# Optimization experiments

Hardware: AMD Instinct MI355X
Metric: run time of the kernel (lower is better)

## Reference

```python
import jax, jax.numpy as jnp
import numpy as np

EPS = 1e-5
K = 20

def knn_idx(x, k):
    # x: (B, N, C). Torch computes -||xi-xj||^2 and takes topk (largest => nearest).
    xx = jnp.sum(x * x, axis=-1)                      # (B, N)
    inner = jnp.einsum('bnc,bmc->bnm', x, x)          # (B, N, N)
    neg_dist = 2.0 * inner - xx[:, :, None] - xx[:, None, :]
    return jax.lax.top_k(neg_dist, k)[1]              # (B, N, k) int32

def edge_feature(x, k):
    # x: (B, N, C) -> (B, N, k, 2C) = concat(neighbor - center, center)
    B = x.shape[0]
    idx = knn_idx(x, k)
    nb = x[jnp.arange(B)[:, None, None], idx]         # (B, N, k, C) gather
    ctr = jnp.broadcast_to(x[:, :, None, :], nb.shape)
    return jnp.concatenate([nb - ctr, ctr], axis=-1)

def batchnorm(x, gamma, beta, axes):
    # training-mode BN over `axes` (per-channel on last axis)
    m = jnp.mean(x, axis=axes, keepdims=True)
    v = jnp.var(x, axis=axes, keepdims=True)
    return (x - m) * jax.lax.rsqrt(v + EPS) * gamma + beta

def lrelu(x):
    return jnp.where(x >= 0, x, 0.2 * x)

def conv_bn_act(x, w, g, b):
    # 1x1 conv on (B, N, k, Cin) with weight (Cout, Cin), BN over (B, N, k)
    y = jnp.einsum('bnkc,oc->bnko', x, w)
    return lrelu(batchnorm(y, g, b, (0, 1, 2)))


def setup_inputs() -> dict:
    key = jax.random.key(0)
    ks = jax.random.split(key, 16)
    B, N = 4, 4096
    d = {'x': jax.random.normal(ks[0], (B, 3, N), dtype=jnp.float32)}
    d['w1'] = jax.random.normal(ks[1], (64, 6),    dtype=jnp.float32) * 0.1
    d['w2'] = jax.random.normal(ks[2], (64, 64),   dtype=jnp.float32) * 0.1
    d['w3'] = jax.random.normal(ks[3], (64, 128),  dtype=jnp.float32) * 0.1
    d['w4'] = jax.random.normal(ks[4], (64, 64),   dtype=jnp.float32) * 0.1
    d['w5'] = jax.random.normal(ks[5], (64, 128),  dtype=jnp.float32) * 0.1
    d['w6'] = jax.random.normal(ks[6], (1024, 192), dtype=jnp.float32) * 0.05
    d['wl'] = jax.random.normal(ks[7], (512, 1024), dtype=jnp.float32) * 0.05
    for i, c in zip(range(1, 8), [64, 64, 64, 64, 64, 1024, 512]):
        d[f'g{i}'] = jnp.ones((c,), jnp.float32)
        d[f'b{i}'] = jnp.zeros((c,), jnp.float32)
    return d


def reference(x, w1, w2, w3, w4, w5, w6, wl,
              g1, b1, g2, b2, g3, b3, g4, b4, g5, b5, g6, b6, g7, b7):
    p = jnp.transpose(x[:, :3, :], (0, 2, 1))         # (B, N, 3)
    # EdgeConv block 1
    e = edge_feature(p, K)                            # (B, N, k, 6)
    h = conv_bn_act(e, w1, g1, b1)
    h = conv_bn_act(h, w2, g2, b2)
    x1 = jnp.max(h, axis=2)                           # (B, N, 64)
    # EdgeConv block 2
    e = edge_feature(x1, K)                           # (B, N, k, 128)
    h = conv_bn_act(e, w3, g3, b3)
    h = conv_bn_act(h, w4, g4, b4)
    x2 = jnp.max(h, axis=2)
    # EdgeConv block 3
    e = edge_feature(x2, K)
    h = conv_bn_act(e, w5, g5, b5)
    x3 = jnp.max(h, axis=2)
    # point-wise 1x1 conv to 1024 then global max pool
    cat = jnp.concatenate([x1, x2, x3], axis=-1)      # (B, N, 192)
    h = lrelu(batchnorm(jnp.einsum('bnc,oc->bno', cat, w6), g6, b6, (0, 1)))
    g = jnp.max(h, axis=1)                            # (B, 1024)
    out = batchnorm(g @ wl.T, g7, b7, (0,))           # (B, 512)
    return out
```

## Files before the change

### kernel.cpp

```cpp
#include <hip/hip_runtime.h>

static constexpr int PB  = 4;
static constexpr int PN  = 4096;
static constexpr int PK  = 20;
static constexpr int PNT = PB*PN*PK;
#define NEGF (-3.402823466e38f)

__device__ __forceinline__ float lrelu_f(float x){ return x >= 0.f ? x : 0.2f*x; }

#define FMA4C(accv, av, bv) { accv = fmaf((av).x,(bv).x,accv); accv = fmaf((av).y,(bv).y,accv); \
                              accv = fmaf((av).z,(bv).z,accv); accv = fmaf((av).w,(bv).w,accv); }

__global__ __launch_bounds__(512) void k_knn3(const float* __restrict__ x, int* __restrict__ idxb){
  __shared__ float4 pts[PN];
  int t = threadIdx.x;
  int b = blockIdx.y;
  const float* xb = x + (size_t)b*3*PN;
  for(int i=t;i<PN;i+=512){
    float a0 = xb[i], a1 = xb[PN+i], a2 = xb[2*PN+i];
    float s = a0*a0; s = fmaf(a1,a1,s); s = fmaf(a2,a2,s);
    pts[i] = make_float4(a0,a1,a2,s);
  }
  __syncthreads();
  int lane = t & 63, w = t >> 6;
  int row = blockIdx.x*8 + w;
  float4 pi = pts[row];
  unsigned long long removed = 0ull;

#define KDIST(E) ({ float4 pj_ = pts[lane + ((E)<<6)]; \
    float dt_ = pi.x*pj_.x; dt_ = fmaf(pi.y,pj_.y,dt_); dt_ = fmaf(pi.z,pj_.z,dt_); \
    fmaf(2.f,dt_,-pi.w) - pj_.w; })

  float gv0,gv1,gv2,gv3,gv4,gv5,gv6,gv7;
  int   gi0,gi1,gi2,gi3,gi4,gi5,gi6,gi7;
#define KBUILDG(G) { float gm_=NEGF; int ge_=(G)*8; \
    _Pragma("unroll") for(int e_=(G)*8; e_<(G)*8+8; e_++){ \
      bool ok_ = ((removed >> e_) & 1ull) == 0ull; \
      float d_ = KDIST(e_); \
      bool bt_ = ok_ && (d_ > gm_); gm_ = bt_ ? d_ : gm_; ge_ = bt_ ? e_ : ge_; } \
    gv##G = gm_; gi##G = ge_; }
  KBUILDG(0) KBUILDG(1) KBUILDG(2) KBUILDG(3) KBUILDG(4) KBUILDG(5) KBUILDG(6) KBUILDG(7)

  float lmax; int le;
#define KLBEST { lmax = gv0; le = gi0; \
    if(gv1>lmax){lmax=gv1;le=gi1;} if(gv2>lmax){lmax=gv2;le=gi2;} \
    if(gv3>lmax){lmax=gv3;le=gi3;} if(gv4>lmax){lmax=gv4;le=gi4;} \
    if(gv5>lmax){lmax=gv5;le=gi5;} if(gv6>lmax){lmax=gv6;le=gi6;} \
    if(gv7>lmax){lmax=gv7;le=gi7;} }
  KLBEST

  int myidx = 0;
  for(int k=0;k<PK;k++){
    float g = lmax;
    #pragma unroll
    for(int s=32;s>=1;s>>=1) g = fmaxf(g, __shfl_xor(g, s));
    unsigned long long cand = __ballot(lmax == g);
    int jw;
    if(__popcll(cand) == 1){
      int wl = __ffsll(cand) - 1;
      int e  = __shfl(le, wl);
      jw = wl + (e<<6);
    } else {
      unsigned jj = (lmax == g) ? (unsigned)(lane + (le<<6)) : 0xFFFFFFFFu;
      #pragma unroll
      for(int s=32;s>=1;s>>=1){ unsigned o = __shfl_xor(jj, s); jj = (o < jj) ? o : jj; }
      jw = (int)jj;
    }
    if(lane == k) myidx = jw;
    if((jw & 63) == lane){
      int e = jw >> 6;
      removed |= (1ull << e);
      int q = e >> 3;
      if(q==0){ KBUILDG(0) } else if(q==1){ KBUILDG(1) }
      else if(q==2){ KBUILDG(2) } else if(q==3){ KBUILDG(3) }
      else if(q==4){ KBUILDG(4) } else if(q==5){ KBUILDG(5) }
      else if(q==6){ KBUILDG(6) } else { KBUILDG(7) }
      KLBEST
    }
  }
  if(lane < PK) idxb[((size_t)b*PN + row)*PK + lane] = myidx;
#undef KDIST
#undef KBUILDG
#undef KLBEST
}

__global__ __launch_bounds__(256) void k_dist64(const float* __restrict__ Xb, const float* __restrict__ xxb,
                                                float* __restrict__ D){
  __shared__ float Xi[128*32];
  __shared__ float Xj[128*32];
  __shared__ float xxi[128], xxj[128];
  int t = threadIdx.x;
  int p = blockIdx.x;
  int bi = (int)((65.0f - sqrtf(4225.0f - 8.0f*(float)p)) * 0.5f);
  while((bi+1)*32 - ((bi+1)*bi)/2 <= p) bi++;
  while(bi*32 - (bi*(bi-1))/2 > p) bi--;
  int bj = bi + (p - (bi*32 - (bi*(bi-1))/2));
  int i0 = bi*128, j0 = bj*128;
  int prg = t>>4, cq = t&15;
  float acc[8][8];
  #pragma unroll
  for(int pp=0;pp<8;pp++)
    #pragma unroll
    for(int oc=0;oc<8;oc++) acc[pp][oc] = 0.f;

  for(int h=0;h<2;h++){
    if(h) __syncthreads();
    #pragma unroll
    for(int k=0;k<4;k++){
      int fid = t + k*256; int row = fid>>3, c4 = fid&7;
      ((float4*)Xi)[row*8 + (c4^(row&7))] = ((const float4*)(Xb + (size_t)(i0+row)*64 + h*32))[c4];
      ((float4*)Xj)[row*8 + (c4^(row&7))] = ((const float4*)(Xb + (size_t)(j0+row)*64 + h*32))[c4];
    }
    if(h==0){
      if(t < 128) xxi[t] = xxb[i0+t];
      else        xxj[t-128] = xxb[j0+t-128];
    }
    __syncthreads();
    #pragma unroll 4
    for(int c4=0;c4<8;c4++){
      float4 a[8], bb[8];
      #pragma unroll
      for(int pp=0;pp<8;pp++){ int row = prg*8+pp; a[pp] = ((const float4*)Xi)[row*8 + (c4^(row&7))]; }
      #pragma unroll
      for(int oc=0;oc<8;oc++){ int col = cq+16*oc;  bb[oc] = ((const float4*)Xj)[col*8 + (c4^(col&7))]; }
      #pragma unroll
      for(int pp=0;pp<8;pp++)
        #pragma unroll
        for(int oc=0;oc<8;oc++) FMA4C(acc[pp][oc], a[pp], bb[oc]);
    }
  }
  #pragma unroll
  for(int pp=0;pp<8;pp++){
    int r = prg*8+pp;
    float xi2 = xxi[r];
    float* Drow = D + (size_t)(i0+r)*PN + j0;
    #pragma unroll
    for(int oc=0;oc<8;oc++){
      int c = cq + 16*oc;
      Drow[c] = fmaf(2.f, acc[pp][oc], -xi2) - xxj[c];
    }
  }
  if(bi != bj){
    #pragma unroll
    for(int oc=0;oc<8;oc++){
      int c = cq + 16*oc;
      float xj2 = xxj[c];
      float* Dcol = D + (size_t)(j0+c)*PN + i0 + prg*8;
      float4 t0, t1;
      t0.x = fmaf(2.f, acc[0][oc], -xj2) - xxi[prg*8+0];
      t0.y = fmaf(2.f, acc[1][oc], -xj2) - xxi[prg*8+1];
      t0.z = fmaf(2.f, acc[2][oc], -xj2) - xxi[prg*8+2];
      t0.w = fmaf(2.f, acc[3][oc], -xj2) - xxi[prg*8+3];
      t1.x = fmaf(2.f, acc[4][oc], -xj2) - xxi[prg*8+4];
      t1.y = fmaf(2.f, acc[5][oc], -xj2) - xxi[prg*8+5];
      t1.z = fmaf(2.f, acc[6][oc], -xj2) - xxi[prg*8+6];
      t1.w = fmaf(2.f, acc[7][oc], -xj2) - xxi[prg*8+7];
      ((float4*)Dcol)[0] = t0;
      ((float4*)Dcol)[1] = t1;
    }
  }
}

__global__ __launch_bounds__(256) void k_topk(const float* __restrict__ D, int* __restrict__ idxb){
  int t = threadIdx.x, lane = t & 63, w = t >> 6;
  int row = blockIdx.x*4 + w;
  const float4* rp = (const float4*)(D + (size_t)row*PN + lane*64);
  float v[64];
  #pragma unroll
  for(int c=0;c<16;c++){
    float4 q = rp[c];
    v[4*c+0]=q.x; v[4*c+1]=q.y; v[4*c+2]=q.z; v[4*c+3]=q.w;
  }
  float gv0,gv1,gv2,gv3,gv4,gv5,gv6,gv7;
  int   gi0,gi1,gi2,gi3,gi4,gi5,gi6,gi7;
#define TBUILDG(G) { float gm_=NEGF; int ge_=(G)*8; \
    _Pragma("unroll") for(int e_=(G)*8; e_<(G)*8+8; e_++){ \
      bool bt_ = v[e_] > gm_; gm_ = bt_ ? v[e_] : gm_; ge_ = bt_ ? e_ : ge_; } \
    gv##G = gm_; gi##G = ge_; }
#define TPOIS(G) { _Pragma("unroll") for(int e_=(G)*8; e_<(G)*8+8; e_++){ \
      if(e_ == rel) v[e_] = NEGF; } }
  TBUILDG(0) TBUILDG(1) TBUILDG(2) TBUILDG(3) TBUILDG(4) TBUILDG(5) TBUILDG(6) TBUILDG(7)
  float lmax; int li;
#define TLBEST { lmax = gv0; li = gi0; \
    if(gv1>lmax){lmax=gv1;li=gi1;} if(gv2>lmax){lmax=gv2;li=gi2;} \
    if(gv3>lmax){lmax=gv3;li=gi3;} if(gv4>lmax){lmax=gv4;li=gi4;} \
    if(gv5>lmax){lmax=gv5;li=gi5;} if(gv6>lmax){lmax=gv6;li=gi6;} \
    if(gv7>lmax){lmax=gv7;li=gi7;} }
  TLBEST
  int myidx = 0;
  for(int k=0;k<PK;k++){
    float g = lmax;
    #pragma unroll
    for(int s=32;s>=1;s>>=1) g = fmaxf(g, __shfl_xor(g, s));
    unsigned long long mask = __ballot(lmax == g);
    int wl = __ffsll((unsigned long long)mask) - 1;
    int rel = __shfl(li, wl);
    if(lane == k) myidx = wl*64 + rel;
    if(lane == wl){
      int q = rel >> 3;
      if(q==0){ TPOIS(0) TBUILDG(0) } else if(q==1){ TPOIS(1) TBUILDG(1) }
      else if(q==2){ TPOIS(2) TBUILDG(2) } else if(q==3){ TPOIS(3) TBUILDG(3) }
      else if(q==4){ TPOIS(4) TBUILDG(4) } else if(q==5){ TPOIS(5) TBUILDG(5) }
      else if(q==6){ TPOIS(6) TBUILDG(6) } else { TPOIS(7) TBUILDG(7) }
      TLBEST
    }
  }
  if(lane < PK) idxb[row*PK + lane] = myidx;
#undef TBUILDG
#undef TPOIS
#undef TLBEST
}

__global__ __launch_bounds__(256) void k_nodeUV3(const float* __restrict__ x, const float* __restrict__ w1,
                                                 float* __restrict__ U, float* __restrict__ V){
  __shared__ float ww[384];
  int t = threadIdx.x;
  for(int k=t;k<384;k+=256) ww[k] = w1[k];
  __syncthreads();
  int g = blockIdx.x*256 + t;
  int ng = g >> 6, o = g & 63;
  int b = ng >> 12, n = ng & 4095;
  const float* xb = x + (size_t)b*3*PN;
  float p0 = xb[n], p1 = xb[PN+n], p2 = xb[2*PN+n];
  const float* wr = ww + o*6;
  float u = p0*wr[0]; u = fmaf(p1,wr[1],u); u = fmaf(p2,wr[2],u);
  float vv = p0*(wr[3]-wr[0]); vv = fmaf(p1, wr[4]-wr[1], vv); vv = fmaf(p2, wr[5]-wr[2], vv);
  U[(size_t)ng*64+o] = u;
  V[(size_t)ng*64+o] = vv;
}

__global__ __launch_bounds__(256) void k_nodeUV64(const float* __restrict__ xf, const float* __restrict__ w,
                                                  float* __restrict__ U, float* __restrict__ V){
  __shared__ float xbuf[128*64];
  __shared__ float wbuf[128*64];
  int t = threadIdx.x;
  int r0 = blockIdx.x * 128;
  #pragma unroll
  for(int k=0;k<8;k++){
    int fid = t + k*256; int row = fid>>4, c4 = fid&15;
    ((float4*)xbuf)[row*16 + (c4^(row&15))] = ((const float4*)(xf + (size_t)(r0+row)*64))[c4];
    float4 wv;
    if(row < 64){
      wv = ((const float4*)(w + (size_t)row*128))[c4];
    } else {
      float4 w2v = ((const float4*)(w + (size_t)(row-64)*128 + 64))[c4];
      float4 w1v = ((const float4*)(w + (size_t)(row-64)*128))[c4];
      wv.x = w2v.x-w1v.x; wv.y = w2v.y-w1v.y; wv.z = w2v.z-w1v.z; wv.w = w2v.w-w1v.w;
    }
    ((float4*)wbuf)[row*16 + (c4^(row&15))] = wv;
  }
  __syncthreads();
  int rg = t>>4, cq = t&15;
  float acc[8][8];
  #pragma unroll
  for(int pp=0;pp<8;pp++)
    #pragma unroll
    for(int oc=0;oc<8;oc++) acc[pp][oc] = 0.f;
  #pragma unroll 4
  for(int c4=0;c4<16;c4++){
    float4 a[8], bb[8];
    #pragma unroll
    for(int pp=0;pp<8;pp++){ int row = rg*8+pp; a[pp] = ((const float4*)xbuf)[row*16 + (c4^(row&15))]; }
    #pragma unroll
    for(int oc=0;oc<8;oc++){ int col = cq+16*oc;  bb[oc] = ((const float4*)wbuf)[col*16 + (c4^(col&15))]; }
    #pragma unroll
    for(int pp=0;pp<8;pp++)
      #pragma unroll
      for(int oc=0;oc<8;oc++) FMA4C(acc[pp][oc], a[pp], bb[oc]);
  }
  #pragma unroll
  for(int pp=0;pp<8;pp++){
    int r = r0 + rg*8+pp;
    #pragma unroll
    for(int oc=0;oc<8;oc++){
      int col = cq + 16*oc;
      if(col < 64) U[(size_t)r*64 + col] = acc[pp][oc];
      else         V[(size_t)r*64 + col-64] = acc[pp][oc];
    }
  }
}

__global__ __launch_bounds__(256) void k_statUV(const float* __restrict__ U, const float* __restrict__ V,
                                                const int* __restrict__ idx, float* __restrict__ part){
  __shared__ float4 sArr[256];
  __shared__ float4 qArr[256];
  int t = threadIdx.x; int blk = blockIdx.x;
  int ch4 = t & 15, sub = t >> 4;
  int qbase = blk*640;
  float4 s = make_float4(0,0,0,0), qq = make_float4(0,0,0,0);
  for(int r=sub; r<640; r+=16){
    int q = qbase + r;
    int pt = q/PK;
    int b = pt >> 12;
    int j = idx[q];
    float4 u4 = ((const float4*)(U + (size_t)(b*PN+j)*64))[ch4];
    float4 v4 = ((const float4*)(V + (size_t)pt*64))[ch4];
    float4 y4;
    y4.x = u4.x+v4.x; y4.y = u4.y+v4.y; y4.z = u4.z+v4.z; y4.w = u4.w+v4.w;
    s.x += y4.x; s.y += y4.y; s.z += y4.z; s.w += y4.w;
    qq.x = fmaf(y4.x,y4.x,qq.x); qq.y = fmaf(y4.y,y4.y,qq.y);
    qq.z = fmaf(y4.z,y4.z,qq.z); qq.w = fmaf(y4.w,y4.w,qq.w);
  }
  sArr[t] = s; qArr[t] = qq;
  __syncthreads();
  if(t < 16){
    float4 S = make_float4(0,0,0,0), Q = make_float4(0,0,0,0);
    #pragma unroll
    for(int g=0;g<16;g++){
      float4 a = sArr[g*16 + t], b = qArr[g*16 + t];
      S.x+=a.x; S.y+=a.y; S.z+=a.z; S.w+=a.w;
      Q.x+=b.x; Q.y+=b.y; Q.z+=b.z; Q.w+=b.w;
    }
    ((float4*)(part + (size_t)blk*128))[t] = S;
    ((float4*)(part + (size_t)blk*128 + 64))[t] = Q;
  }
}

__global__ __launch_bounds__(256) void k_convAF(const float* __restrict__ U, const float* __restrict__ V,
                                                const int* __restrict__ idx, const float* __restrict__ wg,
                                                const float* __restrict__ sb, float* __restrict__ y,
                                                float* __restrict__ part){
  __shared__ float hbuf[128*64];
  __shared__ float wbuf[64*64];
  int t = threadIdx.x;
  int q0 = blockIdx.x * 128;
  #pragma unroll
  for(int k=0;k<8;k++){
    int fid = t + k*256; int row = fid>>4, c4 = fid&15;
    int q = q0 + row;
    int pt = q/PK; int b = pt>>12; int j = idx[q];
    float4 uu = ((const float4*)(U + (size_t)(b*PN+j)*64))[c4];
    float4 vv = ((const float4*)(V + (size_t)pt*64))[c4];
    float4 sc = ((const float4*)sb)[c4];
    float4 bi = ((const float4*)(sb+1024))[c4];
    float4 h;
    h.x = lrelu_f(fmaf(uu.x+vv.x, sc.x, bi.x));
    h.y = lrelu_f(fmaf(uu.y+vv.y, sc.y, bi.y));
    h.z = lrelu_f(fmaf(uu.z+vv.z, sc.z, bi.z));
    h.w = lrelu_f(fmaf(uu.w+vv.w, sc.w, bi.w));
    ((float4*)hbuf)[row*16 + (c4 ^ (row&15))] = h;
  }
  #pragma unroll
  for(int k=0;k<4;k++){
    int fid = t + k*256; int row = fid>>4, c4 = fid&15;
    ((float4*)wbuf)[row*16 + (c4 ^ (row&15))] = ((const float4*)(wg + row*64))[c4];
  }
  __syncthreads();
  int prg = t >> 4, cq = t & 15;
  float acc[8][4];
  #pragma unroll
  for(int pp=0;pp<8;pp++)
    #pragma unroll
    for(int oc=0;oc<4;oc++) acc[pp][oc] = 0.f;
  #pragma unroll 4
  for(int c4=0;c4<16;c4++){
    float4 a[8], b4[4];
    #pragma unroll
    for(int pp=0;pp<8;pp++){ int row = prg*8+pp; a[pp] = ((const float4*)hbuf)[row*16 + (c4^(row&15))]; }
    #pragma unroll
    for(int oc=0;oc<4;oc++){ int och = cq + 16*oc; b4[oc] = ((const float4*)wbuf)[och*16 + (c4^(och&15))]; }
    #pragma unroll
    for(int pp=0;pp<8;pp++)
      #pragma unroll
      for(int oc=0;oc<4;oc++) FMA4C(acc[pp][oc], a[pp], b4[oc]);
  }
  #pragma unroll
  for(int pp=0;pp<8;pp++)
    #pragma unroll
    for(int oc=0;oc<4;oc++)
      y[(size_t)(q0 + prg*8+pp)*64 + cq + 16*oc] = acc[pp][oc];

  float s_[4], q_[4];
  #pragma unroll
  for(int oc=0;oc<4;oc++){
    float s = 0.f, q = 0.f;
    #pragma unroll
    for(int pp=0;pp<8;pp++){ s += acc[pp][oc]; q = fmaf(acc[pp][oc], acc[pp][oc], q); }
    s_[oc] = s; q_[oc] = q;
  }
  __syncthreads();
  float* ls = wbuf;
  #pragma unroll
  for(int oc=0;oc<4;oc++){
    ls[(cq + 16*oc)*16 + prg]        = s_[oc];
    ls[2048 + (cq + 16*oc)*16 + prg] = q_[oc];
  }
  __syncthreads();
  if(t < 64){
    float S = 0.f, Q = 0.f;
    #pragma unroll
    for(int g=0;g<16;g++){ S += ls[t*16+g]; Q += ls[2048 + t*16+g]; }
    part[(size_t)blockIdx.x*128 + t] = S;
    part[(size_t)blockIdx.x*128 + 64 + t] = Q;
  }
}

__global__ __launch_bounds__(256) void k_red1024(const float* __restrict__ y6, float* __restrict__ part){
  int t = threadIdx.x; int blk = blockIdx.x;
  const float4* base = (const float4*)(y6 + (size_t)blk*128*1024);
  float4 s = make_float4(0,0,0,0), q = make_float4(0,0,0,0);
  for(int r=0;r<128;r++){
    float4 v = base[r*256 + t];
    s.x += v.x; s.y += v.y; s.z += v.z; s.w += v.w;
    q.x = fmaf(v.x,v.x,q.x); q.y = fmaf(v.y,v.y,q.y); q.z = fmaf(v.z,v.z,q.z); q.w = fmaf(v.w,v.w,q.w);
  }
  ((float4*)(part + (size_t)blk*2048))[t] = s;
  ((float4*)(part + (size_t)blk*2048 + 1024))[t] = q;
}

__global__ __launch_bounds__(256) void k_fin(const float* __restrict__ part, int nparts, int chn, float cnt,
                                             const float* __restrict__ gamma, const float* __restrict__ beta,
                                             float* __restrict__ sb){
  __shared__ float ls[512];
  int t = threadIdx.x;
  int chl = t & 15, sub = t >> 4;
  int ch = blockIdx.x*16 + chl;
  float S = 0.f, Q = 0.f;
  for(int p=sub; p<nparts; p+=16){
    S += part[(size_t)p*2*chn + ch];
    Q += part[(size_t)p*2*chn + chn + ch];
  }
  ls[t] = S; ls[256+t] = Q;
  __syncthreads();
  if(t < 16){
    float Sa = 0.f, Qa = 0.f;
    #pragma unroll
    for(int s=0;s<16;s++){ Sa += ls[s*16+t]; Qa += ls[256+s*16+t]; }
    int c = blockIdx.x*16 + t;
    float m  = Sa/cnt;
    float vr = Qa/cnt - m*m;
    float sc = gamma[c] * rsqrtf(vr + 1e-5f);
    sb[c] = sc; sb[1024+c] = beta[c] - m*sc;
  }
}

__global__ __launch_bounds__(256) void k_finish(const float* __restrict__ y, const float* __restrict__ sb,
                                                float* __restrict__ xo, float* __restrict__ xxo){
  __shared__ float ls[256];
  int t = threadIdx.x;
  int pt = blockIdx.x*16 + (t>>4), c4 = t&15;
  const float4* base = (const float4*)(y + (size_t)pt*20*64);
  float4 sc = ((const float4*)sb)[c4];
  float4 bi = ((const float4*)(sb+1024))[c4];
  float4 m = make_float4(NEGF,NEGF,NEGF,NEGF);
  #pragma unroll 4
  for(int k=0;k<20;k++){
    float4 v = base[k*16 + c4];
    v.x = lrelu_f(fmaf(v.x, sc.x, bi.x)); v.y = lrelu_f(fmaf(v.y, sc.y, bi.y));
    v.z = lrelu_f(fmaf(v.z, sc.z, bi.z)); v.w = lrelu_f(fmaf(v.w, sc.w, bi.w));
    m.x = fmaxf(m.x,v.x); m.y = fmaxf(m.y,v.y); m.z = fmaxf(m.z,v.z); m.w = fmaxf(m.w,v.w);
  }
  ((float4*)(xo + (size_t)pt*64))[c4] = m;
  float ss = m.x*m.x; ss = fmaf(m.y,m.y,ss); ss = fmaf(m.z,m.z,ss); ss = fmaf(m.w,m.w,ss);
  ls[t] = ss;
  __syncthreads();
  if(c4 == 0){
    float S = 0.f;
    #pragma unroll
    for(int c=0;c<16;c++) S += ls[(t & 0xF0) + c];
    xxo[pt] = S;
  }
}

__global__ __launch_bounds__(256) void k_finishUV(const float* __restrict__ U, const float* __restrict__ V,
                                                  const int* __restrict__ idx, const float* __restrict__ sb,
                                                  float* __restrict__ xo){
  int t = threadIdx.x;
  int pt = blockIdx.x*16 + (t>>4), c4 = t&15;
  int b = pt >> 12;
  float4 sc = ((const float4*)sb)[c4];
  float4 bi = ((const float4*)(sb+1024))[c4];
  float4 vv = ((const float4*)(V + (size_t)pt*64))[c4];
  float4 m = make_float4(NEGF,NEGF,NEGF,NEGF);
  const int* ip = idx + (size_t)pt*PK;
  #pragma unroll 4
  for(int k=0;k<PK;k++){
    int j = ip[k];
    float4 uu = ((const float4*)(U + (size_t)(b*PN+j)*64))[c4];
    float4 v;
    v.x = lrelu_f(fmaf(uu.x+vv.x, sc.x, bi.x)); v.y = lrelu_f(fmaf(uu.y+vv.y, sc.y, bi.y));
    v.z = lrelu_f(fmaf(uu.z+vv.z, sc.z, bi.z)); v.w = lrelu_f(fmaf(uu.w+vv.w, sc.w, bi.w));
    m.x = fmaxf(m.x,v.x); m.y = fmaxf(m.y,v.y); m.z = fmaxf(m.z,v.z); m.w = fmaxf(m.w,v.w);
  }
  ((float4*)(xo + (size_t)pt*64))[c4] = m;
}

__global__ __launch_bounds__(256) void k_gemm6(const float* __restrict__ x1, const float* __restrict__ x2,
                                               const float* __restrict__ x3, const float* __restrict__ w6,
                                               float* __restrict__ y6){
  __shared__ float cb[128*64];
  __shared__ float wb[128*64];
  int t = threadIdx.x;
  int rb = blockIdx.x >> 3;
  int ob = blockIdx.x & 7;
  size_t r0 = (size_t)rb*128; int o0 = ob*128;
  int prg = t >> 4, cq = t & 15;
  float acc[8][8];
  #pragma unroll
  for(int pp=0;pp<8;pp++)
    #pragma unroll
    for(int oc=0;oc<8;oc++) acc[pp][oc] = 0.f;
  const float* srcs[3] = {x1, x2, x3};
  for(int ph=0; ph<3; ph++){
    __syncthreads();
    const float* src = srcs[ph];
    #pragma unroll
    for(int k=0;k<8;k++){
      int fid = t + k*256; int row = fid>>4, c4 = fid&15;
      ((float4*)cb)[row*16 + (c4^(row&15))] = ((const float4*)(src + (r0+row)*64))[c4];
      ((float4*)wb)[row*16 + (c4^(row&15))] = ((const float4*)(w6 + (size_t)(o0+row)*192 + ph*64))[c4];
    }
    __syncthreads();
    #pragma unroll 4
    for(int c4=0;c4<16;c4++){
      float4 a[8], b8[8];
      #pragma unroll
      for(int pp=0;pp<8;pp++){ int row = prg*8+pp; a[pp] = ((const float4*)cb)[row*16 + (c4^(row&15))]; }
      #pragma unroll
      for(int oc=0;oc<8;oc++){ int och = cq + 16*oc; b8[oc] = ((const float4*)wb)[och*16 + (c4^(och&15))]; }
      #pragma unroll
      for(int pp=0;pp<8;pp++)
        #pragma unroll
        for(int oc=0;oc<8;oc++) FMA4C(acc[pp][oc], a[pp], b8[oc]);
    }
  }
  #pragma unroll
  for(int pp=0;pp<8;pp++)
    #pragma unroll
    for(int oc=0;oc<8;oc++)
      y6[(r0 + prg*8+pp)*1024 + o0 + cq + 16*oc] = acc[pp][oc];
}

__global__ __launch_bounds__(256) void k_gmax(const float* __restrict__ y6, const float* __restrict__ sb,
                                              float* __restrict__ gpart){
  int t = threadIdx.x; int blk = blockIdx.x;
  const float4* base = (const float4*)(y6 + (size_t)blk*256*1024);
  float4 sc = ((const float4*)sb)[t];
  float4 bi = ((const float4*)(sb+1024))[t];
  float4 m = make_float4(NEGF,NEGF,NEGF,NEGF);
  for(int r=0;r<256;r++){
    float4 v = base[r*256 + t];
    v.x = lrelu_f(fmaf(v.x, sc.x, bi.x)); v.y = lrelu_f(fmaf(v.y, sc.y, bi.y));
    v.z = lrelu_f(fmaf(v.z, sc.z, bi.z)); v.w = lrelu_f(fmaf(v.w, sc.w, bi.w));
    m.x = fmaxf(m.x,v.x); m.y = fmaxf(m.y,v.y); m.z = fmaxf(m.z,v.z); m.w = fmaxf(m.w,v.w);
  }
  ((float4*)(gpart + (size_t)blk*1024))[t] = m;
}

__global__ __launch_bounds__(256) void k_gmaxfin(const float* __restrict__ gpart, float* __restrict__ g){
  int b = blockIdx.x, t = threadIdx.x;
  float4 m = make_float4(NEGF,NEGF,NEGF,NEGF);
  for(int c=0;c<16;c++){
    float4 v = ((const float4*)(gpart + ((size_t)b*16 + c)*1024))[t];
    m.x = fmaxf(m.x,v.x); m.y = fmaxf(m.y,v.y); m.z = fmaxf(m.z,v.z); m.w = fmaxf(m.w,v.w);
  }
  ((float4*)(g + (size_t)b*1024))[t] = m;
}

__global__ __launch_bounds__(256) void k_final(const float* __restrict__ g, const float* __restrict__ wl,
                                               const float* __restrict__ g7, const float* __restrict__ b7,
                                               float* __restrict__ out){
  int gt = blockIdx.x*256 + threadIdx.x;
  int o = gt >> 2, b = gt & 3;
  const float4* gb = (const float4*)(g + (size_t)b*1024);
  const float4* wr = (const float4*)(wl + (size_t)o*1024);
  float acc = 0.f;
  #pragma unroll 4
  for(int c=0;c<256;c++){
    float4 a = gb[c], w = wr[c];
    acc = fmaf(a.x,w.x,acc); acc = fmaf(a.y,w.y,acc);
    acc = fmaf(a.z,w.z,acc); acc = fmaf(a.w,w.w,acc);
  }
  float s = acc + __shfl_xor(acc, 1);
  s = s + __shfl_xor(s, 2);
  float m = s * 0.25f;
  float d = acc - m;
  float vv = d*d;
  float v2 = vv + __shfl_xor(vv, 1);
  v2 = v2 + __shfl_xor(v2, 2);
  float var = v2 * 0.25f;
  out[b*512 + o] = d * rsqrtf(var + 1e-5f) * g7[o] + b7[o];
}

extern "C" void kernel_launch(void* const* d_in, const int* in_sizes, int n_in,
                              void* d_out, int out_size, void* d_ws, size_t ws_size,
                              hipStream_t stream){
  const float* x  = (const float*)d_in[0];
  const float* w1 = (const float*)d_in[1];
  const float* w2 = (const float*)d_in[2];
  const float* w3 = (const float*)d_in[3];
  const float* w4 = (const float*)d_in[4];
  const float* w5 = (const float*)d_in[5];
  const float* w6 = (const float*)d_in[6];
  const float* wl = (const float*)d_in[7];
  const float* g1 = (const float*)d_in[8];  const float* b1 = (const float*)d_in[9];
  const float* g2 = (const float*)d_in[10]; const float* b2 = (const float*)d_in[11];
  const float* g3 = (const float*)d_in[12]; const float* b3 = (const float*)d_in[13];
  const float* g4 = (const float*)d_in[14]; const float* b4 = (const float*)d_in[15];
  const float* g5 = (const float*)d_in[16]; const float* b5 = (const float*)d_in[17];
  const float* g6 = (const float*)d_in[18]; const float* b6 = (const float*)d_in[19];
  const float* g7 = (const float*)d_in[20]; const float* b7 = (const float*)d_in[21];
  float* out = (float*)d_out;

  float* ws    = (float*)d_ws;
  float* xx    = ws;
  int*   idx   = (int*)(ws + 16384);
  float* y     = ws + 344064;
  float* Dbuf  = y;
  float* x1    = ws + 21315584;
  float* x2    = x1 + 1048576;
  float* x3    = x2 + 1048576;
  float* part  = x3 + 1048576;
  float* sb    = part + 327680;
  float* gpart = sb + 2048;
  float* g     = gpart + 65536;
  float* U     = g + 4096;
  float* V     = U + 1048576;

  k_knn3<<<dim3(512,4),512,0,stream>>>(x, idx);
  k_nodeUV3<<<4096,256,0,stream>>>(x, w1, U, V);
  k_statUV<<<512,256,0,stream>>>(U, V, idx, part);
  k_fin<<<4,256,0,stream>>>(part, 512, 64, (float)PNT, g1, b1, sb);
  k_convAF<<<2560,256,0,stream>>>(U, V, idx, w2, sb, y, part);
  k_fin<<<4,256,0,stream>>>(part, 2560, 64, (float)PNT, g2, b2, sb);
  k_finish<<<1024,256,0,stream>>>(y, sb, x1, xx);

  for(int b=0;b<PB;b++){
    k_dist64<<<528,256,0,stream>>>(x1 + (size_t)b*PN*64, xx + b*PN, Dbuf);
    k_topk<<<1024,256,0,stream>>>(Dbuf, idx + (size_t)b*PN*PK);
  }
  k_nodeUV64<<<128,256,0,stream>>>(x1, w3, U, V);
  k_statUV<<<512,256,0,stream>>>(U, V, idx, part);
  k_fin<<<4,256,0,stream>>>(part, 512, 64, (float)PNT, g3, b3, sb);
  k_convAF<<<2560,256,0,stream>>>(U, V, idx, w4, sb, y, part);
  k_fin<<<4,256,0,stream>>>(part, 2560, 64, (float)PNT, g4, b4, sb);
  k_finish<<<1024,256,0,stream>>>(y, sb, x2, xx);

  for(int b=0;b<PB;b++){
    k_dist64<<<528,256,0,stream>>>(x2 + (size_t)b*PN*64, xx + b*PN, Dbuf);
    k_topk<<<1024,256,0,stream>>>(Dbuf, idx + (size_t)b*PN*PK);
  }
  k_nodeUV64<<<128,256,0,stream>>>(x2, w5, U, V);
  k_statUV<<<512,256,0,stream>>>(U, V, idx, part);
  k_fin<<<4,256,0,stream>>>(part, 512, 64, (float)PNT, g5, b5, sb);
  k_finishUV<<<1024,256,0,stream>>>(U, V, idx, sb, x3);

  k_gemm6<<<1024,256,0,stream>>>(x1, x2, x3, w6, y);
  k_red1024<<<128,256,0,stream>>>(y, part);
  k_fin<<<64,256,0,stream>>>(part, 128, 1024, 16384.f, g6, b6, sb);
  k_gmax<<<64,256,0,stream>>>(y, sb, gpart);
  k_gmaxfin<<<4,256,0,stream>>>(gpart, g);
  k_final<<<8,256,0,stream>>>(g, wl, g7, b7, out);
}
```

Before: 1.245 ms.

## Use split-bf16 MFMA for the 64x64 edge conv GEMM in k_convAF

Replaces the scalar FP32 FMA inner product in k_convAF with bf16 MFMA instructions (16x16x32). Inputs and weights are split into hi and lo bf16 parts and combined with three MFMAs per tile, which approximates FP32 accuracy. Shared-memory staging changes to a swizzled bf16 layout. The goal is to offload the GEMM to the matrix cores, at the cost of extra conversion work and slightly lower precision than true FP32.

Result: faster. 1.199 ms (-3.7%).

```diff
diff --git a/kernel.cpp b/kernel.cpp
--- a/kernel.cpp
+++ b/kernel.cpp
@@ -7,6 +7,16 @@
 #define NEGF (-3.402823466e38f)
 
 __device__ __forceinline__ float lrelu_f(float x){ return x >= 0.f ? x : 0.2f*x; }
+
+typedef __attribute__((ext_vector_type(8))) short short8v;
+typedef __attribute__((ext_vector_type(4))) float f32x4;
+
+__device__ __forceinline__ unsigned short f2bf(float f){
+  unsigned u = __float_as_uint(f);
+  unsigned r = u + 0x7FFFu + ((u>>16)&1u);
+  return (unsigned short)(r>>16);
+}
+__device__ __forceinline__ float bf2f(unsigned short s){ return __uint_as_float(((unsigned)s)<<16); }
 
 #define FMA4C(accv, av, bv) { accv = fmaf((av).x,(bv).x,accv); accv = fmaf((av).y,(bv).y,accv); \
                               accv = fmaf((av).z,(bv).z,accv); accv = fmaf((av).w,(bv).w,accv); }
@@ -320,8 +330,8 @@
                                                 const int* __restrict__ idx, const float* __restrict__ wg,
                                                 const float* __restrict__ sb, float* __restrict__ y,
                                                 float* __restrict__ part){
-  __shared__ float hbuf[128*64];
-  __shared__ float wbuf[64*64];
+  __shared__ short hb[2*128*64];
+  __shared__ short wb[2*64*64];
   int t = threadIdx.x;
   int q0 = blockIdx.x * 128;
   #pragma unroll
@@ -338,52 +348,95 @@
     h.y = lrelu_f(fmaf(uu.y+vv.y, sc.y, bi.y));
     h.z = lrelu_f(fmaf(uu.z+vv.z, sc.z, bi.z));
     h.w = lrelu_f(fmaf(uu.w+vv.w, sc.w, bi.w));
-    ((float4*)hbuf)[row*16 + (c4 ^ (row&15))] = h;
+    int base = row*64 + ((((c4>>1) ^ (row&7)))<<3) + ((c4&1)<<2);
+    short4 hi4, lo4;
+    hi4.x = (short)f2bf(h.x); lo4.x = (short)f2bf(h.x - bf2f((unsigned short)hi4.x));
+    hi4.y = (short)f2bf(h.y); lo4.y = (short)f2bf(h.y - bf2f((unsigned short)hi4.y));
+    hi4.z = (short)f2bf(h.z); lo4.z = (short)f2bf(h.z - bf2f((unsigned short)hi4.z));
+    hi4.w = (short)f2bf(h.w); lo4.w = (short)f2bf(h.w - bf2f((unsigned short)hi4.w));
+    *(short4*)(hb + base) = hi4;
+    *(short4*)(hb + 8192 + base) = lo4;
   }
   #pragma unroll
   for(int k=0;k<4;k++){
     int fid = t + k*256; int row = fid>>4, c4 = fid&15;
-    ((float4*)wbuf)[row*16 + (c4 ^ (row&15))] = ((const float4*)(wg + row*64))[c4];
-  }
-  __syncthreads();
-  int prg = t >> 4, cq = t & 15;
-  float acc[8][4];
-  #pragma unroll
-  for(int pp=0;pp<8;pp++)
-    #pragma unroll
-    for(int oc=0;oc<4;oc++) acc[pp][oc] = 0.f;
-  #pragma unroll 4
-  for(int c4=0;c4<16;c4++){
-    float4 a[8], b4[4];
-    #pragma unroll
-    for(int pp=0;pp<8;pp++){ int row = prg*8+pp; a[pp] = ((const float4*)hbuf)[row*16 + (c4^(row&15))]; }
-    #pragma unroll
-    for(int oc=0;oc<4;oc++){ int och = cq + 16*oc; b4[oc] = ((const float4*)wbuf)[och*16 + (c4^(och&15))]; }
-    #pragma unroll
-    for(int pp=0;pp<8;pp++)
-      #pragma unroll
-      for(int oc=0;oc<4;oc++) FMA4C(acc[pp][oc], a[pp], b4[oc]);
-  }
-  #pragma unroll
-  for(int pp=0;pp<8;pp++)
-    #pragma unroll
-    for(int oc=0;oc<4;oc++)
-      y[(size_t)(q0 + prg*8+pp)*64 + cq + 16*oc] = acc[pp][oc];
-
-  float s_[4], q_[4];
-  #pragma unroll
-  for(int oc=0;oc<4;oc++){
-    float s = 0.f, q = 0.f;
-    #pragma unroll
-    for(int pp=0;pp<8;pp++){ s += acc[pp][oc]; q = fmaf(acc[pp][oc], acc[pp][oc], q); }
-    s_[oc] = s; q_[oc] = q;
-  }
-  __syncthreads();
-  float* ls = wbuf;
-  #pragma unroll
-  for(int oc=0;oc<4;oc++){
-    ls[(cq + 16*oc)*16 + prg]        = s_[oc];
-    ls[2048 + (cq + 16*oc)*16 + prg] = q_[oc];
+    float4 wv = ((const float4*)(wg + (size_t)row*64))[c4];
+    int base = row*64 + ((((c4>>1) ^ (row&7)))<<3) + ((c4&1)<<2);
+    short4 hi4, lo4;
+    hi4.x = (short)f2bf(wv.x); lo4.x = (short)f2bf(wv.x - bf2f((unsigned short)hi4.x));
+    hi4.y = (short)f2bf(wv.y); lo4.y = (short)f2bf(wv.y - bf2f((unsigned short)hi4.y));
+    hi4.z = (short)f2bf(wv.z); lo4.z = (short)f2bf(wv.z - bf2f((unsigned short)hi4.z));
+    hi4.w = (short)f2bf(wv.w); lo4.w = (short)f2bf(wv.w - bf2f((unsigned short)hi4.w));
+    *(short4*)(wb + base) = hi4;
+    *(short4*)(wb + 4096 + base) = lo4;
+  }
+  __syncthreads();
+
+  int lane = t & 63, w = t >> 6;
+  int r0w = w*32;
+  short8v ah[2][2], al[2][2];
+  #pragma unroll
+  for(int rt=0;rt<2;rt++)
+    #pragma unroll
+    for(int kc=0;kc<2;kc++){
+      int row = r0w + rt*16 + (lane&15);
+      int kb  = kc*4 + (lane>>4);
+      int off = row*64 + ((kb ^ (row&7))<<3);
+      ah[rt][kc] = *(const short8v*)(hb + off);
+      al[rt][kc] = *(const short8v*)(hb + 8192 + off);
+    }
+  short8v bh[4][2], bl[4][2];
+  #pragma unroll
+  for(int ct=0;ct<4;ct++)
+    #pragma unroll
+    for(int kc=0;kc<2;kc++){
+      int o   = ct*16 + (lane&15);
+      int kb  = kc*4 + (lane>>4);
+      int off = o*64 + ((kb ^ (o&7))<<3);
+      bh[ct][kc] = *(const short8v*)(wb + off);
+      bl[ct][kc] = *(const short8v*)(wb + 4096 + off);
+    }
+
+  f32x4 acc[2][4];
+  #pragma unroll
+  for(int rt=0;rt<2;rt++)
+    #pragma unroll
+    for(int ct=0;ct<4;ct++)
+      acc[rt][ct] = (f32x4){0.f,0.f,0.f,0.f};
+
+  #pragma unroll
+  for(int rt=0;rt<2;rt++)
+    #pragma unroll
+    for(int ct=0;ct<4;ct++)
+      #pragma unroll
+      for(int kc=0;kc<2;kc++){
+        acc[rt][ct] = __builtin_amdgcn_mfma_f32_16x16x32_bf16(ah[rt][kc], bh[ct][kc], acc[rt][ct], 0,0,0);
+        acc[rt][ct] = __builtin_amdgcn_mfma_f32_16x16x32_bf16(ah[rt][kc], bl[ct][kc], acc[rt][ct], 0,0,0);
+        acc[rt][ct] = __builtin_amdgcn_mfma_f32_16x16x32_bf16(al[rt][kc], bh[ct][kc], acc[rt][ct], 0,0,0);
+      }
+
+  float s_[4] = {0.f,0.f,0.f,0.f}, q_[4] = {0.f,0.f,0.f,0.f};
+  #pragma unroll
+  for(int rt=0;rt<2;rt++)
+    #pragma unroll
+    for(int ct=0;ct<4;ct++){
+      int colg = ct*16 + (lane&15);
+      #pragma unroll
+      for(int reg=0;reg<4;reg++){
+        int row = r0w + rt*16 + (lane>>4)*4 + reg;
+        float val = acc[rt][ct][reg];
+        y[(size_t)(q0 + row)*64 + colg] = val;
+        s_[ct] += val; q_[ct] = fmaf(val, val, q_[ct]);
+      }
+    }
+
+  __syncthreads();
+  float* ls = (float*)wb;
+  #pragma unroll
+  for(int ct=0;ct<4;ct++){
+    int colg = ct*16 + (lane&15);
+    ls[colg*16 + (w*4 + (lane>>4))]        = s_[ct];
+    ls[2048 + colg*16 + (w*4 + (lane>>4))] = q_[ct];
   }
   __syncthreads();
   if(t < 64){
@@ -489,7 +542,7 @@
                                                const float* __restrict__ x3, const float* __restrict__ w6,
                                                float* __restrict__ y6){
   __shared__ float cb[128*64];
-  __shared__ float wb[128*64];
+  __shared__ float wb2[128*64];
   int t = threadIdx.x;
   int rb = blockIdx.x >> 3;
   int ob = blockIdx.x & 7;
@@ -508,7 +561,7 @@
     for(int k=0;k<8;k++){
       int fid = t + k*256; int row = fid>>4, c4 = fid&15;
       ((float4*)cb)[row*16 + (c4^(row&15))] = ((const float4*)(src + (r0+row)*64))[c4];
-      ((float4*)wb)[row*16 + (c4^(row&15))] = ((const float4*)(w6 + (size_t)(o0+row)*192 + ph*64))[c4];
+      ((float4*)wb2)[row*16 + (c4^(row&15))] = ((const float4*)(w6 + (size_t)(o0+row)*192 + ph*64))[c4];
     }
     __syncthreads();
     #pragma unroll 4
@@ -517,7 +570,7 @@
       #pragma unroll
       for(int pp=0;pp<8;pp++){ int row = prg*8+pp; a[pp] = ((const float4*)cb)[row*16 + (c4^(row&15))]; }
       #pragma unroll
-      for(int oc=0;oc<8;oc++){ int och = cq + 16*oc; b8[oc] = ((const float4*)wb)[och*16 + (c4^(och&15))]; }
+      for(int oc=0;oc<8;oc++){ int och = cq + 16*oc; b8[oc] = ((const float4*)wb2)[och*16 + (c4^(och&15))]; }
       #pragma unroll
       for(int pp=0;pp<8;pp++)
         #pragma unroll
```
